# Optimization experiments

Hardware: AMD Instinct MI355X
Metric: run time of the kernel (lower is better)

## Reference

```python
import jax, jax.numpy as jnp
import numpy as np


def setup_inputs() -> dict:
    key = jax.random.key(0)
    k_x, k_pos, k_val, k_temp = jax.random.split(key, 4)
    B, T, D, N = 8, 2048, 512, 4096
    x = jax.random.normal(k_x, (B, T, D), dtype=jnp.float32)
    # module init: positions ~ N(0,1)*0.5, values ~ N(0,1)*0.02
    positions = jax.random.normal(k_pos, (N, D), dtype=jnp.float32) * 0.5
    values = jax.random.normal(k_val, (N, D), dtype=jnp.float32) * 0.02
    # 'trained' temperatures ~ U[4,6] so the RBF kernel does not underflow at D=512
    temperature = 4.0 + 2.0 * jax.random.uniform(k_temp, (N,), dtype=jnp.float32)
    # neuron_scale buffer at late-tide level (MAX_SCALE = 0.8)
    neuron_scale = jnp.full((N,), 0.8, dtype=jnp.float32)
    return {"x": x, "positions": positions, "values": values,
            "temperature": temperature, "neuron_scale": neuron_scale}


def reference(x, positions, values, temperature, neuron_scale):
    B, T, D = x.shape
    x_flat = x.reshape(-1, D)                                  # [M, D], M = B*T
    x_sq = jnp.sum(x_flat * x_flat, axis=-1, keepdims=True)    # [M, 1]
    p_sq = jnp.sum(positions * positions, axis=-1)             # [N]
    cross = x_flat @ positions.T                               # [M, N] GEMM
    dists = jnp.sqrt(jnp.maximum(x_sq + p_sq[None, :] - 2.0 * cross, 0.0))
    effective_temp = (jnp.abs(temperature) + 0.1) * neuron_scale  # [N]
    weights = jnp.exp(-dists / effective_temp[None, :])        # [M, N]
    weights = weights / (jnp.sum(weights, axis=-1, keepdims=True) + 1e-8)
    out = weights @ values                                     # [M, D] GEMM
    return out.reshape(B, T, D)
```

## Files before the change

kernel.cpp:

```cpp
#include <hip/hip_runtime.h>
#include <hip/hip_bf16.h>

typedef __attribute__((ext_vector_type(8))) short short8;
typedef __attribute__((ext_vector_type(4))) float f32x4;
typedef __attribute__((ext_vector_type(4))) unsigned short u16x4;

__device__ __forceinline__ unsigned short f2bf(float f) {
  union { float f; unsigned u; } v; v.f = f;
  unsigned r = v.u + 0x7fffu + ((v.u >> 16) & 1u);
  return (unsigned short)(r >> 16);
}

template <int EPI, int WM, int WN, int MI, int BK, int NBUF>
__global__ __launch_bounds__(WM * WN * 64, 2) void rbf_gemm(
    const unsigned short* __restrict__ A, const unsigned short* __restrict__ Bt,
    int Ncols, int K,
    const float* __restrict__ xsq, const float* __restrict__ psq,
    const float* __restrict__ rtemp, unsigned short* __restrict__ Wout,
    float* __restrict__ part, int Mtot, const float* __restrict__ denin,
    float* __restrict__ outp, int row0, int ldOut) {
  constexpr int NT = WM * WN * 64;
  constexpr int BM = WM * MI * 16;
  constexpr int BN = WN * 64;
  constexpr int CH = BK / 8;
  constexpr int CMASK = CH - 1;
  constexpr int AIT = BM * CH / NT;
  constexpr int BIT = BN * CH / NT;
  constexpr int LOADS = AIT + BIT;
  constexpr int DEPTH = NBUF - 1;
  constexpr int KS = BK / 32;
  constexpr int ASZ = BM * BK;
  constexpr int TSZ = (BM + BN) * BK;
  constexpr int BOUNCE = EPI == 1 ? BM * BN * 2 : BM * BN;
  constexpr int SELEMS = NBUF * TSZ > BOUNCE ? NBUF * TSZ : BOUNCE;
  __shared__ __align__(16) unsigned short smem[SELEMS];

  const int t = threadIdx.x;
  const int lane = t & 63, wid = t >> 6;
  const int wm = wid / WN, wn = wid % WN;
  const int lr = lane & 15, lg = lane >> 4;

  int bm, bn;
  {
    int swz = blockIdx.x;
    if (EPI == 0) {
      const int nb = Ncols / BN;
      const int nwg = gridDim.x;
      if ((nwg & 7) == 0) {
        int cpx = nwg >> 3;
        swz = (swz & 7) * cpx + (swz >> 3);
      }
      bm = swz / nb;
      bn = swz - bm * nb;
    } else {
      const int nbm = gridDim.x / (Ncols / BN);
      bm = swz % nbm;
      bn = swz / nbm;
    }
  }

  const unsigned short* Ab = A + (size_t)bm * BM * K;
  const unsigned short* Bb = Bt + (size_t)bn * BN * K;

  const unsigned short* gA[AIT];
  const unsigned short* gB[BIT];
#pragma unroll
  for (int i = 0; i < AIT; ++i) {
    const int idx = i * NT + t;
    const int r = idx / CH, c = idx & CMASK;
    gA[i] = Ab + (size_t)r * K + ((c ^ (r & CMASK)) << 3);
  }
#pragma unroll
  for (int i = 0; i < BIT; ++i) {
    const int idx = i * NT + t;
    const int r = idx / CH, c = idx & CMASK;
    gB[i] = Bb + (size_t)r * K + ((c ^ (r & CMASK)) << 3);
  }
  const int dwave = wid << 9;

  int offA[MI][KS], offB[4][KS];
#pragma unroll
  for (int mi = 0; mi < MI; ++mi) {
    const int ar = wm * (MI * 16) + mi * 16 + lr;
#pragma unroll
    for (int ks = 0; ks < KS; ++ks)
      offA[mi][ks] = ar * BK + ((((ks << 2) | lg) ^ (ar & CMASK)) << 3);
  }
#pragma unroll
  for (int ni = 0; ni < 4; ++ni) {
    const int br = wn * 64 + ni * 16 + lr;
#pragma unroll
    for (int ks = 0; ks < KS; ++ks)
      offB[ni][ks] = ASZ + br * BK + ((((ks << 2) | lg) ^ (br & CMASK)) << 3);
  }

  f32x4 acc[MI][4];
#pragma unroll
  for (int i = 0; i < MI; ++i)
#pragma unroll
    for (int j = 0; j < 4; ++j) acc[i][j] = (f32x4){0.f, 0.f, 0.f, 0.f};

#define STAGE(step, bufi)                                                              \
  do {                                                                                 \
    const int ko = (step) * BK;                                                        \
    const int bo = (bufi) * TSZ;                                                       \
    _Pragma("unroll")                                                                  \
    for (int i = 0; i < AIT; ++i)                                                      \
      __builtin_amdgcn_global_load_lds(                                                \
          (const __attribute__((address_space(1))) void*)(gA[i] + ko),                 \
          (__attribute__((address_space(3))) void*)(smem + bo + i * (NT * 8) + dwave), \
          16, 0, 0);                                                                   \
    _Pragma("unroll")                                                                  \
    for (int i = 0; i < BIT; ++i)                                                      \
      __builtin_amdgcn_global_load_lds(                                                \
          (const __attribute__((address_space(1))) void*)(gB[i] + ko),                 \
          (__attribute__((address_space(3))) void*)(smem + bo + ASZ + i * (NT * 8) + dwave), \
          16, 0, 0);                                                                   \
  } while (0)

  const int nsteps = K / BK;
#pragma unroll
  for (int p = 0; p < DEPTH; ++p)
    if (p < nsteps) STAGE(p, p);

  int bc = 0, bp = DEPTH % NBUF;
  for (int s = 0; s < nsteps; ++s) {
    if (s + DEPTH < nsteps) {
      STAGE(s + DEPTH, bp);
      asm volatile("s_waitcnt vmcnt(%0)" :: "i"(DEPTH * LOADS) : "memory");
    } else if (DEPTH >= 2 && s + 1 < nsteps) {
      asm volatile("s_waitcnt vmcnt(%0)" :: "i"(LOADS) : "memory");
    } else {
      asm volatile("s_waitcnt vmcnt(0)" ::: "memory");
    }
    __builtin_amdgcn_s_barrier();
    const unsigned short* sb = smem + bc * TSZ;
    __builtin_amdgcn_s_setprio(1);
#pragma unroll
    for (int ks = 0; ks < KS; ++ks) {
      short8 af[MI], bf[4];
#pragma unroll
      for (int mi = 0; mi < MI; ++mi) af[mi] = *(const short8*)&sb[offA[mi][ks]];
#pragma unroll
      for (int ni = 0; ni < 4; ++ni) bf[ni] = *(const short8*)&sb[offB[ni][ks]];
#pragma unroll
      for (int mi = 0; mi < MI; ++mi)
#pragma unroll
        for (int ni = 0; ni < 4; ++ni)
          acc[mi][ni] = __builtin_amdgcn_mfma_f32_16x16x32_bf16(af[mi], bf[ni],
                                                                acc[mi][ni], 0, 0, 0);
    }
    __builtin_amdgcn_s_setprio(0);
    asm volatile("s_waitcnt lgkmcnt(0)" ::: "memory");
    __builtin_amdgcn_s_barrier();
    bc = bc + 1 == NBUF ? 0 : bc + 1;
    bp = bp + 1 == NBUF ? 0 : bp + 1;
  }
#undef STAGE

  if (EPI == 0) {
    float ps[4], rt[4];
#pragma unroll
    for (int ni = 0; ni < 4; ++ni) {
      const int col = bn * BN + wn * 64 + ni * 16 + lr;
      ps[ni] = psq[col];
      rt[ni] = rtemp[col];
    }
    float* slice = part + (size_t)(bn * WN + wn) * Mtot;
#pragma unroll
    for (int mi = 0; mi < MI; ++mi) {
#pragma unroll
      for (int j = 0; j < 4; ++j) {
        const int lrow = wm * (MI * 16) + mi * 16 + lg * 4 + j;
        const int grow = row0 + bm * BM + lrow;
        const float xq = xsq[grow];
        float rsv = 0.f;
#pragma unroll
        for (int ni = 0; ni < 4; ++ni) {
          const int lcol = wn * 64 + ni * 16 + lr;
          float d2 = xq + ps[ni] - 2.0f * acc[mi][ni][j];
          float dist = __builtin_amdgcn_sqrtf(fmaxf(d2, 0.0f));
          float w = __builtin_amdgcn_exp2f(-dist * rt[ni]);
          smem[lrow * BN + (((lcol >> 3) ^ (lrow & 7)) << 3) + (lcol & 7)] = f2bf(w);
          rsv += w;
        }
        rsv += __shfl_xor(rsv, 1);
        rsv += __shfl_xor(rsv, 2);
        rsv += __shfl_xor(rsv, 4);
        rsv += __shfl_xor(rsv, 8);
        if (lr == 0) slice[grow] = rsv;
      }
    }
    __syncthreads();
    constexpr int HB = BN / 8;
#pragma unroll
    for (int i = 0; i < BM * BN / 8 / NT; ++i) {
      const int id = i * NT + t;
      const int r = id / HB, h = id % HB;
      short8 v = *(const short8*)&smem[r * BN + ((h ^ (r & 7)) << 3)];
      *(short8*)&Wout[(size_t)(bm * BM + r) * ldOut + bn * BN + h * 8] = v;
    }
  } else {
    float* smemf = (float*)smem;
#pragma unroll
    for (int mi = 0; mi < MI; ++mi)
#pragma unroll
      for (int j = 0; j < 4; ++j) {
        const int lrow = wm * (MI * 16) + mi * 16 + lg * 4 + j;
#pragma unroll
        for (int ni = 0; ni < 4; ++ni) {
          const int lcol = wn * 64 + ni * 16 + lr;
          smemf[lrow * BN + (((lcol >> 2) ^ (lrow & 7)) << 2) + (lcol & 3)] =
              acc[mi][ni][j];
        }
      }
    __syncthreads();
    constexpr int HB4 = BN / 4;
#pragma unroll
    for (int i = 0; i < BM * BN / 4 / NT; ++i) {
      const int id = i * NT + t;
      const int r = id / HB4, h = id % HB4;
      const int grow = row0 + bm * BM + r;
      const float rd = 1.0f / (denin[grow] + 1e-8f);
      f32x4 v = *(const f32x4*)&smemf[r * BN + ((h ^ (r & 7)) << 2)];
      v *= rd;
      __builtin_nontemporal_store(v,
          (f32x4*)&outp[(size_t)grow * ldOut + bn * BN + h * 4]);
    }
  }
}

__global__ void reduce_denom(const float* __restrict__ part, float* __restrict__ denom,
                             int Mtot, int row0, int S) {
  const int m = row0 + blockIdx.x * 128 + threadIdx.x;
  float s = 0.f;
  for (int i = 0; i < S; ++i) s += part[(size_t)i * Mtot + m];
  denom[m] = s;
}

__global__ void prep_rows(const float* __restrict__ in, unsigned short* __restrict__ outb,
                          float* __restrict__ sq, int D) {
  const int row = blockIdx.x;
  const int t = threadIdx.x;
  const float4 v = ((const float4*)(in + (size_t)row * D))[t];
  u16x4 o = {f2bf(v.x), f2bf(v.y), f2bf(v.z), f2bf(v.w)};
  *(u16x4*)(outb + (size_t)row * D + t * 4) = o;
  float s = v.x * v.x + v.y * v.y + v.z * v.z + v.w * v.w;
  for (int off = 32; off; off >>= 1) s += __shfl_xor(s, off);
  __shared__ float ws[16];
  if ((t & 63) == 0) ws[t >> 6] = s;
  __syncthreads();
  if (t == 0) {
    float tot = 0.f;
    const int nw = blockDim.x >> 6;
    for (int i = 0; i < nw; ++i) tot += ws[i];
    sq[row] = tot;
  }
}

__global__ void prep_scale(const float* __restrict__ tmp, const float* __restrict__ sc,
                           float* __restrict__ rtemp, int N) {
  const int i = blockIdx.x * blockDim.x + threadIdx.x;
  if (i < N) rtemp[i] = 1.4426950408889634f / ((fabsf(tmp[i]) + 0.1f) * sc[i]);
}

__global__ void prep_vT(const float* __restrict__ vals, unsigned short* __restrict__ vT,
                        int N, int D) {
  __shared__ float tile[32][33];
  const int nt = blockIdx.x, dt = blockIdx.y;
  const int tx = threadIdx.x, ty = threadIdx.y;
#pragma unroll
  for (int i = 0; i < 4; ++i) {
    int r = nt * 32 + ty + i * 8;
    tile[ty + i * 8][tx] = vals[(size_t)r * D + dt * 32 + tx];
  }
  __syncthreads();
#pragma unroll
  for (int i = 0; i < 4; ++i) {
    int d = dt * 32 + ty + i * 8;
    vT[(size_t)d * N + nt * 32 + tx] = f2bf(tile[tx][ty + i * 8]);
  }
}

extern "C" void kernel_launch(void* const* d_in, const int* in_sizes, int n_in,
                              void* d_out, int out_size, void* d_ws, size_t ws_size,
                              hipStream_t stream) {
  const float* x = (const float*)d_in[0];
  const float* pos = (const float*)d_in[1];
  const float* vals = (const float*)d_in[2];
  const float* temp = (const float*)d_in[3];
  const float* nsc = (const float*)d_in[4];
  float* out = (float*)d_out;

  const int N = in_sizes[3];
  const int D = in_sizes[1] / N;
  const int M = in_sizes[0] / D;
  const int S = 2 * (N / 128);

  char* ws = (char*)d_ws;
  size_t off = 0;
  auto alloc = [&](size_t bytes) {
    void* p = ws + off;
    off = (off + bytes + 255) & ~(size_t)255;
    return p;
  };
  unsigned short* xb = (unsigned short*)alloc((size_t)M * D * 2);
  unsigned short* pb = (unsigned short*)alloc((size_t)N * D * 2);
  unsigned short* vT = (unsigned short*)alloc((size_t)D * N * 2);
  float* xsq = (float*)alloc((size_t)M * 4);
  float* psq = (float*)alloc((size_t)N * 4);
  float* rtemp = (float*)alloc((size_t)N * 4);
  float* denom = (float*)alloc((size_t)M * 4);
  float* part = (float*)alloc((size_t)S * M * 4);

  size_t avail = ws_size > off ? ws_size - off : 0;
  long long mc_ll = (long long)(avail / ((size_t)N * 2));
  int Mc = (int)((mc_ll / 128) * 128);
  if (Mc > M) Mc = M;
  if (Mc < 128) Mc = 128;
  unsigned short* W = (unsigned short*)alloc((size_t)Mc * N * 2);

  prep_rows<<<M, D / 4, 0, stream>>>(x, xb, xsq, D);
  prep_rows<<<N, D / 4, 0, stream>>>(pos, pb, psq, D);
  prep_scale<<<(N + 255) / 256, 256, 0, stream>>>(temp, nsc, rtemp, N);
  dim3 tg(N / 32, D / 32);
  prep_vT<<<tg, dim3(32, 8), 0, stream>>>(vals, vT, N, D);

  for (int row0 = 0; row0 < M; row0 += Mc) {
    const int mc = (M - row0) < Mc ? (M - row0) : Mc;
    const int g1 = (mc / 128) * (N / 128);
    rbf_gemm<0, 2, 2, 4, 64, 2><<<g1, 256, 0, stream>>>(
        xb + (size_t)row0 * D, pb, N, D, xsq, psq, rtemp, W, part, M,
        nullptr, nullptr, row0, N);
    reduce_denom<<<mc / 128, 128, 0, stream>>>(part, denom, M, row0, S);
    const int g2 = (mc / 128) * (D / 256);
    rbf_gemm<1, 2, 4, 4, 64, 2><<<g2, 512, 0, stream>>>(
        W, vT, D, N, nullptr, nullptr, nullptr, nullptr,
        part, M, denom, out, row0, D);
  }
}
```

Measured before the change: 238.2 us.

## Raise occupancy target and retile distance GEMM to 512-thread blocks

Raises the launch-bounds occupancy hint from 2 to 4 blocks per CU. The first (distance) GEMM moves from 4 waves with 4 M-fragments each to 8 waves (4x2) with 2 fragments each, keeping the same 128x128 block tile. The XCD-aware block swizzle for the first GEMM is dropped in favour of plain column-major block mapping. The double-buffer loop is rewritten with pointer bumps and an XOR buffer offset; with NBUF=2 this behaves like the old loop. The tighter register budget raises spill risk, most of all in the second GEMM, which still keeps 64 accumulator floats per thread at 512 threads. Losing the swizzle may also cut L2 locality across XCDs.

Measured after the change: 210.3 us. 1.13x faster.

```diff
diff --git a/kernel.cpp b/kernel.cpp
--- a/kernel.cpp
+++ b/kernel.cpp
@@ -12,7 +12,7 @@
 }
 
 template <int EPI, int WM, int WN, int MI, int BK, int NBUF>
-__global__ __launch_bounds__(WM * WN * 64, 2) void rbf_gemm(
+__global__ __launch_bounds__(WM * WN * 64, 4) void rbf_gemm(
     const unsigned short* __restrict__ A, const unsigned short* __restrict__ Bt,
     int Ncols, int K,
     const float* __restrict__ xsq, const float* __restrict__ psq,
@@ -27,7 +27,6 @@
   constexpr int AIT = BM * CH / NT;
   constexpr int BIT = BN * CH / NT;
   constexpr int LOADS = AIT + BIT;
-  constexpr int DEPTH = NBUF - 1;
   constexpr int KS = BK / 32;
   constexpr int ASZ = BM * BK;
   constexpr int TSZ = (BM + BN) * BK;
@@ -40,24 +39,9 @@
   const int wm = wid / WN, wn = wid % WN;
   const int lr = lane & 15, lg = lane >> 4;
 
-  int bm, bn;
-  {
-    int swz = blockIdx.x;
-    if (EPI == 0) {
-      const int nb = Ncols / BN;
-      const int nwg = gridDim.x;
-      if ((nwg & 7) == 0) {
-        int cpx = nwg >> 3;
-        swz = (swz & 7) * cpx + (swz >> 3);
-      }
-      bm = swz / nb;
-      bn = swz - bm * nb;
-    } else {
-      const int nbm = gridDim.x / (Ncols / BN);
-      bm = swz % nbm;
-      bn = swz / nbm;
-    }
-  }
+  const int nbm = gridDim.x / (Ncols / BN);
+  const int bm = blockIdx.x % nbm;
+  const int bn = blockIdx.x / nbm;
 
   const unsigned short* Ab = A + (size_t)bm * BM * K;
   const unsigned short* Bb = Bt + (size_t)bn * BN * K;
@@ -100,41 +84,38 @@
 #pragma unroll
     for (int j = 0; j < 4; ++j) acc[i][j] = (f32x4){0.f, 0.f, 0.f, 0.f};
 
-#define STAGE(step, bufi)                                                              \
+#define STAGE(bo)                                                                      \
   do {                                                                                 \
-    const int ko = (step) * BK;                                                        \
-    const int bo = (bufi) * TSZ;                                                       \
     _Pragma("unroll")                                                                  \
-    for (int i = 0; i < AIT; ++i)                                                      \
+    for (int i = 0; i < AIT; ++i) {                                                    \
       __builtin_amdgcn_global_load_lds(                                                \
-          (const __attribute__((address_space(1))) void*)(gA[i] + ko),                 \
-          (__attribute__((address_space(3))) void*)(smem + bo + i * (NT * 8) + dwave), \
+          (const __attribute__((address_space(1))) void*)gA[i],                        \
+          (__attribute__((address_space(3))) void*)(smem + (bo) + i * (NT * 8) + dwave), \
           16, 0, 0);                                                                   \
+      gA[i] += BK;                                                                     \
+    }                                                                                  \
     _Pragma("unroll")                                                                  \
-    for (int i = 0; i < BIT; ++i)                                                      \
+    for (int i = 0; i < BIT; ++i) {                                                    \
       __builtin_amdgcn_global_load_lds(                                                \
-          (const __attribute__((address_space(1))) void*)(gB[i] + ko),                 \
-          (__attribute__((address_space(3))) void*)(smem + bo + ASZ + i * (NT * 8) + dwave), \
+          (const __attribute__((address_space(1))) void*)gB[i],                        \
+          (__attribute__((address_space(3))) void*)(smem + (bo) + ASZ + i * (NT * 8) + dwave), \
           16, 0, 0);                                                                   \
+      gB[i] += BK;                                                                     \
+    }                                                                                  \
   } while (0)
 
   const int nsteps = K / BK;
-#pragma unroll
-  for (int p = 0; p < DEPTH; ++p)
-    if (p < nsteps) STAGE(p, p);
-
-  int bc = 0, bp = DEPTH % NBUF;
+  STAGE(0);
+  unsigned buf = 0;
   for (int s = 0; s < nsteps; ++s) {
-    if (s + DEPTH < nsteps) {
-      STAGE(s + DEPTH, bp);
-      asm volatile("s_waitcnt vmcnt(%0)" :: "i"(DEPTH * LOADS) : "memory");
-    } else if (DEPTH >= 2 && s + 1 < nsteps) {
+    if (s + 1 < nsteps) {
+      STAGE(buf ^ TSZ);
       asm volatile("s_waitcnt vmcnt(%0)" :: "i"(LOADS) : "memory");
     } else {
       asm volatile("s_waitcnt vmcnt(0)" ::: "memory");
     }
     __builtin_amdgcn_s_barrier();
-    const unsigned short* sb = smem + bc * TSZ;
+    const unsigned short* sb = smem + buf;
     __builtin_amdgcn_s_setprio(1);
 #pragma unroll
     for (int ks = 0; ks < KS; ++ks) {
@@ -153,8 +134,7 @@
     __builtin_amdgcn_s_setprio(0);
     asm volatile("s_waitcnt lgkmcnt(0)" ::: "memory");
     __builtin_amdgcn_s_barrier();
-    bc = bc + 1 == NBUF ? 0 : bc + 1;
-    bp = bp + 1 == NBUF ? 0 : bp + 1;
+    buf ^= TSZ;
   }
 #undef STAGE
 
@@ -329,7 +309,7 @@
   for (int row0 = 0; row0 < M; row0 += Mc) {
     const int mc = (M - row0) < Mc ? (M - row0) : Mc;
     const int g1 = (mc / 128) * (N / 128);
-    rbf_gemm<0, 2, 2, 4, 64, 2><<<g1, 256, 0, stream>>>(
+    rbf_gemm<0, 4, 2, 2, 64, 2><<<g1, 512, 0, stream>>>(
         xb + (size_t)row0 * D, pb, N, D, xsq, psq, rtemp, W, part, M,
         nullptr, nullptr, row0, N);
     reduce_denom<<<mc / 128, 128, 0, stream>>>(part, denom, M, row0, S);
```
